# Kernel tuning notes

Measured on AMD Instinct MI355X. Metric: run time of the kernel, lower is better.

Reference implementation:

```python
import jax, jax.numpy as jnp
import numpy as np

H = 256
W = 256
CHUNK = 512  # query-point tile size; distance tile is CHUNK x (H*W) = 128 MB fp32
INF = jnp.float32(1e30)


def setup_inputs() -> dict:
    key = jax.random.key(0)
    k1, k2 = jax.random.split(key)
    preds = jax.random.uniform(k1, (H, W), dtype=jnp.float32)
    targets = jax.random.uniform(k2, (H, W), dtype=jnp.float32)
    return {"preds": preds, "targets": targets}


def _directed_hausdorff_sq(coords, mask_a, mask_b):
    """max_{a in A} min_{b in B} ||a-b||^2, tiled over A (online min-max).

    coords: [N,2] float32 pixel coordinates of the full grid
    mask_a/mask_b: [N] bool validity of each grid point in set A / B
    Invalid b -> distance +INF (excluded from the min);
    invalid a -> row min set to -INF (excluded from the max).
    """
    n = coords.shape[0]
    b_sq = jnp.sum(coords * coords, axis=1)  # [N]
    a_chunks = coords.reshape(n // CHUNK, CHUNK, 2)
    ma_chunks = mask_a.reshape(n // CHUNK, CHUNK)

    def body(carry, xs):
        a, ma = xs  # a: [CHUNK,2], ma: [CHUNK]
        a_sq = jnp.sum(a * a, axis=1)  # [CHUNK]
        # squared euclidean distances via |a|^2 + |b|^2 - 2 a.b  -> [CHUNK, N]
        d2 = a_sq[:, None] + b_sq[None, :] - 2.0 * (a @ coords.T)
        d2 = jnp.where(mask_b[None, :], d2, INF)
        row_min = jnp.min(d2, axis=1)              # min over B per query point
        row_min = jnp.where(ma, row_min, -INF)     # drop invalid queries
        return jnp.maximum(carry, jnp.max(row_min)), None

    out, _ = jax.lax.scan(body, -INF, (a_chunks, ma_chunks))
    return out


def reference(preds, targets):
    ys, xs = jnp.meshgrid(jnp.arange(H), jnp.arange(W), indexing="ij")
    coords = jnp.stack([ys.ravel(), xs.ravel()], axis=1).astype(jnp.float32)  # [H*W, 2]
    mp = preds.ravel() > 0.5
    mt = targets.ravel() > 0.5
    d_fwd = _directed_hausdorff_sq(coords, mp, mt)   # pred -> target
    d_bwd = _directed_hausdorff_sq(coords, mt, mp)   # target -> pred
    # symmetric Hausdorff = max of the two directed distances; sqrt is monotone
    return jnp.sqrt(jnp.maximum(jnp.maximum(d_fwd, d_bwd), 0.0))
```

## Files before the change

### kernel.cpp

```cpp
#include <hip/hip_runtime.h>
#include <math.h>

#define H 256
#define W 256

__global__ __launch_bounds__(1024) void hd_all(const float* __restrict__ preds,
                                               const float* __restrict__ targets,
                                               float* __restrict__ out) {
    const int b = blockIdx.x;
    const int dir = b >> 6;
    const int x0 = (b & 63) * 4;
    const float* Asrc = dir ? targets : preds;
    const float* Bsrc = dir ? preds : targets;

    const int t = threadIdx.x;
    const int col = t >> 8;
    const int y = t & (H - 1);
    const int xq = x0 + col;

    const float aq = Asrc[y * W + xq];

    __shared__ unsigned long long rmT[4][H];
    __shared__ float gsP[4][3 * H];
    __shared__ float wmax[16];

    {
        const int w = t >> 6, l = t & 63;
        const float4* B4 = (const float4*)Bsrc;
#pragma unroll 4
        for (int i = 0; i < 16; ++i) {
            const int yy = (w << 4) + i;
            const float4 f = B4[yy * (W / 4) + l];
            const unsigned long long m0 = __ballot(f.x > 0.5f);
            const unsigned long long m1 = __ballot(f.y > 0.5f);
            const unsigned long long m2 = __ballot(f.z > 0.5f);
            const unsigned long long m3 = __ballot(f.w > 0.5f);
            if (l == 0) {
                rmT[0][yy] = m0; rmT[1][yy] = m1;
                rmT[2][yy] = m2; rmT[3][yy] = m3;
            }
        }
    }
    gsP[col][y] = 1e30f;
    gsP[col][512 + y] = 1e30f;
    __syncthreads();

    int best = 1 << 20;
#pragma unroll
    for (int j = 0; j < 4; ++j) {
        const unsigned long long v = rmT[j][y];
        const int tt = xq - j;
        const int kL = (tt >= 0) ? (tt >> 2) : -1;
        const int kR = (tt <= 0) ? 0 : ((tt + 3) >> 2);
        const unsigned long long mlo =
            (kL >= 63) ? ~0ull : ((kL < 0) ? 0ull : ((1ull << (kL + 1)) - 1ull));
        const unsigned long long mhi =
            (kR >= 64) ? 0ull : ((kR <= 0) ? ~0ull : ~((1ull << kR) - 1ull));
        const unsigned long long lo = v & mlo;
        const unsigned long long hi = v & mhi;
        if (lo) best = min(best, xq - (((63 - __clzll((long long)lo)) << 2) + j));
        if (hi) best = min(best, (((__ffsll((long long)hi) - 1) << 2) + j) - xq);
    }
    gsP[col][256 + y] = (best >= (1 << 20)) ? 1e30f : (float)(best * best);
    __syncthreads();

    const float* gsr = &gsP[col][256];
    float best2 = gsr[y];
    for (int k = 1; k < 256; ++k) {
        const float kf = (float)k;
        const float kk = kf * kf;
        if (__all(kk >= best2)) break;
        best2 = fminf(best2, kk + fminf(gsr[y - k], gsr[y + k]));
    }

    float v = (aq > 0.5f) ? best2 : 0.0f;

    for (int off = 32; off; off >>= 1) v = fmaxf(v, __shfl_down(v, off, 64));
    if ((t & 63) == 0) wmax[t >> 6] = v;
    __syncthreads();
    if (t == 0) {
        float bm = wmax[0];
#pragma unroll
        for (int i = 1; i < 16; ++i) bm = fmaxf(bm, wmax[i]);
        atomicMax((int*)out, __float_as_int(sqrtf(bm)));
    }
}

extern "C" void kernel_launch(void* const* d_in, const int* in_sizes, int n_in,
                              void* d_out, int out_size, void* d_ws, size_t ws_size,
                              hipStream_t stream) {
    const float* preds = (const float*)d_in[0];
    const float* targets = (const float*)d_in[1];
    float* out = (float*)d_out;
    hd_all<<<128, 1024, 0, stream>>>(preds, targets, out);
}
```

Measured before the change: 13.23 us.

## Use 32-column local window bitmask per block with global-row fallback search

Each block now covers 2 query columns with 512 threads across 256 blocks. Instead of ballot-transposing the whole B image into full-row bitmasks, it loads only a 32-column window around the query columns. It finds the nearest row hit inside that window with clz/ffs, and falls back to a linear scan of the global row when the window cannot bound the distance. This cuts the per-block mask-building load and LDS traffic and doubles block count for better CU spread, at the cost of a divergent fallback loop when a window holds no nearby set pixel.

```diff
diff --git a/kernel.cpp b/kernel.cpp
--- a/kernel.cpp
+++ b/kernel.cpp
@@ -4,12 +4,12 @@
 #define H 256
 #define W 256
 
-__global__ __launch_bounds__(1024) void hd_all(const float* __restrict__ preds,
-                                               const float* __restrict__ targets,
-                                               float* __restrict__ out) {
+__global__ __launch_bounds__(512) void hd_all(const float* __restrict__ preds,
+                                              const float* __restrict__ targets,
+                                              float* __restrict__ out) {
     const int b = blockIdx.x;
-    const int dir = b >> 6;
-    const int x0 = (b & 63) * 4;
+    const int dir = b >> 7;
+    const int x0 = (b & 127) * 2;
     const float* Asrc = dir ? targets : preds;
     const float* Bsrc = dir ? preds : targets;
 
@@ -17,71 +17,78 @@
     const int col = t >> 8;
     const int y = t & (H - 1);
     const int xq = x0 + col;
+    const int xw0 = min(max(x0 - 15, 0), W - 32);
 
     const float aq = Asrc[y * W + xq];
 
-    __shared__ unsigned long long rmT[4][H];
-    __shared__ float gsP[4][3 * H];
-    __shared__ float wmax[16];
+    __shared__ unsigned wm[H];
+    __shared__ alignas(16) float gsP[2][3 * H];
+    __shared__ float wmax[8];
+
+    gsP[col][y] = 1e30f;
+    gsP[col][512 + y] = 1e30f;
 
     {
-        const int w = t >> 6, l = t & 63;
-        const float4* B4 = (const float4*)Bsrc;
-#pragma unroll 4
+        const int w = t >> 6;
+#pragma unroll
         for (int i = 0; i < 16; ++i) {
-            const int yy = (w << 4) + i;
-            const float4 f = B4[yy * (W / 4) + l];
-            const unsigned long long m0 = __ballot(f.x > 0.5f);
-            const unsigned long long m1 = __ballot(f.y > 0.5f);
-            const unsigned long long m2 = __ballot(f.z > 0.5f);
-            const unsigned long long m3 = __ballot(f.w > 0.5f);
-            if (l == 0) {
-                rmT[0][yy] = m0; rmT[1][yy] = m1;
-                rmT[2][yy] = m2; rmT[3][yy] = m3;
+            const int e = t + 512 * i;
+            const int r = e >> 5;
+            const int c = e & 31;
+            const float f = Bsrc[r * W + xw0 + c];
+            const unsigned long long bal = __ballot(f > 0.5f);
+            if ((t & 63) == 0) {
+                const int r0 = 2 * w + 16 * i;
+                wm[r0] = (unsigned)bal;
+                wm[r0 + 1] = (unsigned)(bal >> 32);
             }
         }
     }
-    gsP[col][y] = 1e30f;
-    gsP[col][512 + y] = 1e30f;
     __syncthreads();
 
-    int best = 1 << 20;
-#pragma unroll
-    for (int j = 0; j < 4; ++j) {
-        const unsigned long long v = rmT[j][y];
-        const int tt = xq - j;
-        const int kL = (tt >= 0) ? (tt >> 2) : -1;
-        const int kR = (tt <= 0) ? 0 : ((tt + 3) >> 2);
-        const unsigned long long mlo =
-            (kL >= 63) ? ~0ull : ((kL < 0) ? 0ull : ((1ull << (kL + 1)) - 1ull));
-        const unsigned long long mhi =
-            (kR >= 64) ? 0ull : ((kR <= 0) ? ~0ull : ~((1ull << kR) - 1ull));
-        const unsigned long long lo = v & mlo;
-        const unsigned long long hi = v & mhi;
-        if (lo) best = min(best, xq - (((63 - __clzll((long long)lo)) << 2) + j));
-        if (hi) best = min(best, (((__ffsll((long long)hi) - 1) << 2) + j) - xq);
+    const int rq = xq - xw0;
+    const unsigned v = wm[y];
+    const unsigned mlo = (rq == 31) ? 0xffffffffu : ((2u << rq) - 1u);
+    const unsigned lov = v & mlo;
+    const unsigned hiv = v & ~((1u << rq) - 1u);
+    int bestd = 1 << 20;
+    if (lov) bestd = rq - 31 + __clz(lov);
+    if (hiv) bestd = min(bestd, (__ffs(hiv) - 1) - rq);
+
+    const bool lfull = (xw0 == 0);
+    const bool rfull = (xw0 == W - 32);
+    const int ub = min(lfull ? (1 << 20) : rq + 1,
+                       rfull ? (1 << 20) : 32 - rq);
+    if (bestd > ub) {
+        const float* rowB = Bsrc + y * W;
+        bestd = 1 << 20;
+        for (int k = 1; k < W; ++k) {
+            const int xl = xq - k, xr = xq + k;
+            const bool hit = (xl >= 0 && rowB[xl] > 0.5f) ||
+                             (xr < W && rowB[xr] > 0.5f);
+            if (hit) { bestd = k; break; }
+        }
     }
-    gsP[col][256 + y] = (best >= (1 << 20)) ? 1e30f : (float)(best * best);
+    gsP[col][256 + y] = (bestd >= (1 << 20)) ? 1e30f : (float)(bestd * bestd);
     __syncthreads();
 
     const float* gsr = &gsP[col][256];
     float best2 = gsr[y];
     for (int k = 1; k < 256; ++k) {
-        const float kf = (float)k;
-        const float kk = kf * kf;
+        const float kk = (float)(k * k);
         if (__all(kk >= best2)) break;
         best2 = fminf(best2, kk + fminf(gsr[y - k], gsr[y + k]));
     }
 
-    float v = (aq > 0.5f) ? best2 : 0.0f;
+    float vv = (aq > 0.5f) ? best2 : 0.0f;
 
-    for (int off = 32; off; off >>= 1) v = fmaxf(v, __shfl_down(v, off, 64));
-    if ((t & 63) == 0) wmax[t >> 6] = v;
+    for (int off = 32; off; off >>= 1) vv = fmaxf(vv, __shfl_down(vv, off, 64));
+    if ((t & 63) == 0) wmax[t >> 6] = vv;
     __syncthreads();
     if (t == 0) {
         float bm = wmax[0];
 #pragma unroll
-        for (int i = 1; i < 16; ++i) bm = fmaxf(bm, wmax[i]);
+        for (int i = 1; i < 8; ++i) bm = fmaxf(bm, wmax[i]);
         atomicMax((int*)out, __float_as_int(sqrtf(bm)));
     }
 }
@@ -92,5 +99,5 @@
     const float* preds = (const float*)d_in[0];
     const float* targets = (const float*)d_in[1];
     float* out = (float*)d_out;
-    hd_all<<<128, 1024, 0, stream>>>(preds, targets, out);
+    hd_all<<<256, 512, 0, stream>>>(preds, targets, out);
 }
```

Result: faster. 11.79 us (-10.9%).
